# Kernel optimization log

Measured on AMD Instinct MI355X. Metric: run time of the kernel, lower is better.

The kernel has to match this reference:

```python
import jax, jax.numpy as jnp
import numpy as np

B, N, D, H, DEPTH = 2, 2048, 768, 12, 4
DH = D // H
SCALE = DH ** -0.5
EPS = 1e-5
FF = 4 * D


def layer_norm(x, w, b):
    m = jnp.mean(x, axis=-1, keepdims=True)
    v = jnp.mean((x - m) ** 2, axis=-1, keepdims=True)
    return (x - m) * jax.lax.rsqrt(v + EPS) * w + b


def to_heads(t):  # [b, n, D] -> [b, H, n, DH]
    b, n, _ = t.shape
    return t.reshape(b, n, H, DH).transpose(0, 2, 1, 3)


def merge_heads(t):  # [b, H, n, DH] -> [b, n, D]
    b, h, n, dh = t.shape
    return t.transpose(0, 2, 1, 3).reshape(b, n, D)


def attend(q, k, v, bias):
    s = jnp.einsum('bhid,bhjd->bhij', q, k) * SCALE + bias
    a = jax.nn.softmax(s, axis=-1)
    return merge_heads(jnp.einsum('bhij,bhjd->bhid', a, v))


def setup_inputs():
    key = jax.random.key(0)
    ks = iter(jax.random.split(key, 16))

    def p(shape, scale=0.02):
        return jax.random.normal(next(ks), shape, dtype=jnp.float32) * scale

    inp = {
        'x': jax.random.normal(next(ks), (B, N, D), dtype=jnp.float32),
        'context': jax.random.normal(next(ks), (B, N, D), dtype=jnp.float32),
        'relative_position_bias': jax.random.normal(next(ks), (1, H, N, N), dtype=jnp.float32) * 0.02,
        # self-attn params (stacked over depth)
        'ln1_w': jnp.ones((DEPTH, D), jnp.float32), 'ln1_b': jnp.zeros((DEPTH, D), jnp.float32),
        'w_qkv': p((DEPTH, D, 3 * D)),
        'w_so': p((DEPTH, D, D)), 'b_so': jnp.zeros((DEPTH, D), jnp.float32),
        # cross-attn params (shared LN applied to x and context, as in source)
        'ln2_w': jnp.ones((DEPTH, D), jnp.float32), 'ln2_b': jnp.zeros((DEPTH, D), jnp.float32),
        'w_q': p((DEPTH, D, D)), 'w_k': p((DEPTH, D, D)), 'w_v': p((DEPTH, D, D)),
        'w_co': p((DEPTH, D, D)), 'b_co': jnp.zeros((DEPTH, D), jnp.float32),
        # FFN params
        'ln3_w': jnp.ones((DEPTH, D), jnp.float32), 'ln3_b': jnp.zeros((DEPTH, D), jnp.float32),
        'w_f1': p((DEPTH, D, FF)), 'b_f1': jnp.zeros((DEPTH, FF), jnp.float32),
        'w_f2': p((DEPTH, FF, D)), 'b_f2': jnp.zeros((DEPTH, D), jnp.float32),
        # final norm
        'lnout_w': jnp.ones((D,), jnp.float32), 'lnout_b': jnp.zeros((D,), jnp.float32),
    }
    return inp


def reference(x, context, relative_position_bias,
              ln1_w, ln1_b, w_qkv, w_so, b_so,
              ln2_w, ln2_b, w_q, w_k, w_v, w_co, b_co,
              ln3_w, ln3_b, w_f1, b_f1, w_f2, b_f2,
              lnout_w, lnout_b):
    bias = relative_position_bias
    for i in range(DEPTH):
        # self-attention block (pre-norm, residual)
        xn = layer_norm(x, ln1_w[i], ln1_b[i])
        q, k, v = jnp.split(xn @ w_qkv[i], 3, axis=-1)
        o = attend(to_heads(q), to_heads(k), to_heads(v), bias)
        x = o @ w_so[i] + b_so[i] + x
        # cross-attention block (input_norm shared for x and context)
        xn = layer_norm(x, ln2_w[i], ln2_b[i])
        cn = layer_norm(context, ln2_w[i], ln2_b[i])
        o = attend(to_heads(xn @ w_q[i]), to_heads(cn @ w_k[i]), to_heads(cn @ w_v[i]), bias)
        x = o @ w_co[i] + b_co[i] + x
        # FFN block
        xn = layer_norm(x, ln3_w[i], ln3_b[i])
        h = jax.nn.gelu(xn @ w_f1[i] + b_f1[i], approximate=False)
        x = h @ w_f2[i] + b_f2[i] + x
    return layer_norm(x, lnout_w, lnout_b)
```

## Files before the change

### kernel.cpp

```cpp
#include <hip/hip_runtime.h>
#include <cstdint>
#include <cstddef>

#define DEV static __device__ __forceinline__

typedef float  f32x4 __attribute__((ext_vector_type(4)));
typedef short  s16x8 __attribute__((ext_vector_type(8)));
typedef unsigned short u16;
typedef unsigned short u16x2 __attribute__((ext_vector_type(2)));
typedef unsigned short u16x4 __attribute__((ext_vector_type(4)));
typedef __bf16 bf16x8 __attribute__((ext_vector_type(8)));

#define LOG2E 1.4426950408889634f
#define QSCALE_CONST 0.18033688011112042f

DEV float bf2f(u16 v){ union { unsigned u; float f; } x; x.u = ((unsigned)v) << 16; return x.f; }
DEV u16 f2bf(float f){ return __builtin_bit_cast(u16, (__bf16)f); }

DEV float fexp2(float x){
#if __has_builtin(__builtin_amdgcn_exp2f)
  return __builtin_amdgcn_exp2f(x);
#else
  return exp2f(x);
#endif
}

DEV f32x4 mfma16(s16x8 a, s16x8 b, f32x4 c){
  return __builtin_amdgcn_mfma_f32_16x16x32_bf16(
      __builtin_bit_cast(bf16x8, a), __builtin_bit_cast(bf16x8, b), c, 0, 0, 0);
}

DEV void gld16(const void* g, void* l){
  __builtin_amdgcn_global_load_lds(
      (const __attribute__((address_space(1))) void*)(uintptr_t)g,
      (__attribute__((address_space(3))) void*)(unsigned)(uintptr_t)l,
      16, 0, 0);
}

__global__ void __launch_bounds__(256)
transpose_cvt(const float* __restrict__ src, u16* __restrict__ dst, int K, int N,
              size_t dzstride){
  int z = blockIdx.z;
  src += (size_t)z * K * N;
  dst += (size_t)z * dzstride;
  __shared__ float t[32][33];
  int n0 = blockIdx.x * 32, k0 = blockIdx.y * 32;
#pragma unroll
  for (int i = 0; i < 4; ++i)
    t[threadIdx.y + 8*i][threadIdx.x] = src[(size_t)(k0 + threadIdx.y + 8*i) * N + n0 + threadIdx.x];
  __syncthreads();
#pragma unroll
  for (int i = 0; i < 4; ++i)
    dst[(size_t)(n0 + threadIdx.y + 8*i) * K + k0 + threadIdx.x] = f2bf(t[threadIdx.x][threadIdx.y + 8*i]);
}

__global__ void __launch_bounds__(256)
cvt_bias(const float* __restrict__ in, u16* __restrict__ out){
  size_t i = ((size_t)blockIdx.x * 256 + threadIdx.x) * 4;
  f32x4 v = *(const f32x4*)(in + i);
  u16x4 o;
#pragma unroll
  for (int j = 0; j < 4; ++j) o[j] = f2bf(v[j] * LOG2E);
  *(u16x4*)(out + i) = o;
}

template<typename OUT>
__global__ void __launch_bounds__(256)
ln_kernel(const float* __restrict__ x0, const float* __restrict__ x1,
          const float* __restrict__ w, const float* __restrict__ bsh,
          OUT* __restrict__ o0, OUT* __restrict__ o1){
  int row = blockIdx.x, tid = threadIdx.x;
  const float* xr; OUT* orow;
  if (row < 4096){ xr = x0 + (size_t)row * 768; orow = o0 + (size_t)row * 768; }
  else           { xr = x1 + (size_t)(row - 4096) * 768; orow = o1 + (size_t)(row - 4096) * 768; }
  float v0 = xr[tid], v1 = xr[tid + 256], v2 = xr[tid + 512];
  float s = v0 + v1 + v2, s2 = v0*v0 + v1*v1 + v2*v2;
#pragma unroll
  for (int off = 1; off < 64; off <<= 1){ s += __shfl_xor(s, off); s2 += __shfl_xor(s2, off); }
  __shared__ float red[8];
  int wid = tid >> 6;
  if ((tid & 63) == 0){ red[wid] = s; red[wid + 4] = s2; }
  __syncthreads();
  s  = red[0] + red[1] + red[2] + red[3];
  s2 = red[4] + red[5] + red[6] + red[7];
  float m = s * (1.f/768.f);
  float var = s2 * (1.f/768.f) - m * m;
  float rstd = rsqrtf(var + 1e-5f);
#pragma unroll
  for (int i = 0; i < 3; ++i){
    int c = tid + 256 * i;
    float vv = (i == 0 ? v0 : (i == 1 ? v1 : v2));
    float o = (vv - m) * rstd * w[c] + bsh[c];
    if constexpr (sizeof(OUT) == 2) orow[c] = f2bf(o);
    else                            orow[c] = o;
  }
}

template<int BN, int EPI>
__global__ void __launch_bounds__(256)
gemm_bf16(const u16* __restrict__ A, int lda, const u16* __restrict__ Bt, int ldb,
          int nk, u16* __restrict__ Cb, float* __restrict__ Cf, int ldc,
          const float* __restrict__ bias, const float* __restrict__ resid){
  constexpr int NT = BN / 32;
  __shared__ u16 As[2][128 * 32];
  __shared__ u16 Bs[2][BN * 32];
  const int tid = threadIdx.x, w = tid >> 6, lane = tid & 63;
  const int l16 = lane & 15, g = lane >> 4;
  const int m0 = blockIdx.x * 128, n0 = blockIdx.y * BN;
  const int wm = (w >> 1) * 64, wn = (w & 1) * (BN / 2);
  f32x4 acc[4][NT] = {};

  const int L0 = w * 1024 + lane * 16;
  const int L1 = (w + 4) * 1024 + lane * 16;
  const u16* a0 = A + (size_t)(m0 + (L0 >> 6)) * lda + ((L0 & 63) >> 1);
  const u16* a1 = A + (size_t)(m0 + (L1 >> 6)) * lda + ((L1 & 63) >> 1);
  const u16* b0; const u16* b1 = nullptr;
  if constexpr (BN == 128){
    b0 = Bt + (size_t)(n0 + (L0 >> 6)) * ldb + ((L0 & 63) >> 1);
    b1 = Bt + (size_t)(n0 + (L1 >> 6)) * ldb + ((L1 & 63) >> 1);
  } else {
    const int Lb = tid * 16;
    b0 = Bt + (size_t)(n0 + (Lb >> 6)) * ldb + ((Lb & 63) >> 1);
  }

  {
    char* ab = (char*)As[0]; char* bb = (char*)Bs[0];
    gld16(a0, ab + w * 1024); gld16(a1, ab + (w + 4) * 1024);
    if constexpr (BN == 128){ gld16(b0, bb + w * 1024); gld16(b1, bb + (w + 4) * 1024); }
    else                    { gld16(b0, bb + w * 1024); }
  }
  __syncthreads();

  int cb = 0;
  for (int kt = 0; kt < nk; ++kt){
    if (kt + 1 < nk){
      const int k1 = (kt + 1) * 32;
      char* ab = (char*)As[cb ^ 1]; char* bb = (char*)Bs[cb ^ 1];
      gld16(a0 + k1, ab + w * 1024); gld16(a1 + k1, ab + (w + 4) * 1024);
      if constexpr (BN == 128){ gld16(b0 + k1, bb + w * 1024); gld16(b1 + k1, bb + (w + 4) * 1024); }
      else                    { gld16(b0 + k1, bb + w * 1024); }
    }

    const u16* Ab = As[cb]; const u16* Bb = Bs[cb];
    s16x8 af[4], bfv[NT];
#pragma unroll
    for (int mi = 0; mi < 4; ++mi)
      af[mi] = *(const s16x8*)(Ab + (wm + mi*16 + l16) * 32 + 8 * g);
#pragma unroll
    for (int ni = 0; ni < NT; ++ni)
      bfv[ni] = *(const s16x8*)(Bb + (wn + ni*16 + l16) * 32 + 8 * g);
#pragma unroll
    for (int mi = 0; mi < 4; ++mi)
#pragma unroll
      for (int ni = 0; ni < NT; ++ni)
        acc[mi][ni] = mfma16(af[mi], bfv[ni], acc[mi][ni]);

    __syncthreads();
    cb ^= 1;
  }

#pragma unroll
  for (int mi = 0; mi < 4; ++mi){
    const int rg = m0 + wm + mi*16 + 4*g;
#pragma unroll
    for (int ni = 0; ni < NT; ++ni){
      const int col = n0 + wn + ni*16 + l16;
      f32x4 v = acc[mi][ni];
#pragma unroll
      for (int r = 0; r < 4; ++r){
        const int row = rg + r;
        if constexpr (EPI == 0){
          Cb[(size_t)row * ldc + col] = f2bf(v[r]);
        } else if constexpr (EPI == 1){
          Cf[(size_t)row * ldc + col] = v[r] + bias[col] + resid[(size_t)row * ldc + col];
        } else if constexpr (EPI == 2){
          float t = v[r] + bias[col];
          float ge = 0.5f * t * (1.0f + erff(t * 0.7071067811865476f));
          Cb[(size_t)row * ldc + col] = f2bf(ge);
        } else {
          float sc = (col < 768) ? QSCALE_CONST : 1.0f;
          Cb[(size_t)row * ldc + col] = f2bf(v[r] * sc);
        }
      }
    }
  }
}

__global__ void __launch_bounds__(256)
attn_kernel(const u16* __restrict__ qkv, const u16* __restrict__ bias, u16* __restrict__ out){
  __shared__ __align__(16) u16 Ks [2 * 4096];
  __shared__ __align__(16) u16 Bsh[2 * 4096];
  __shared__ __align__(16) u16 Vt [4096];
  __shared__ __align__(16) u16 Pl [4 * 1024];

  const int tid = threadIdx.x, w = tid >> 6, lane = tid & 63;
  const int l16 = lane & 15, g = lane >> 4;
  const int qt = blockIdx.x, h = blockIdx.y, b = blockIdx.z;
  const int rowbase = b * 2048, q0 = qt * 64;

  const int ci0 = w * 64 + lane, ci1 = ci0 + 256;
  const int r0 = ci0 >> 3, sc0 = ci0 & 7, r1 = ci1 >> 3, sc1 = ci1 & 7;
  const u16* kp0 = qkv + (size_t)(rowbase + r0) * 2304 + 768 + h * 64 + (((sc0 ^ (r0 & 7)) & 7) << 3);
  const u16* kp1 = qkv + (size_t)(rowbase + r1) * 2304 + 768 + h * 64 + (((sc1 ^ (r1 & 7)) & 7) << 3);
  const u16* bp0 = bias + ((size_t)h * 2048 + q0 + r0) * 2048 + (((sc0 ^ (r0 & 7)) & 7) << 3);
  const u16* bp1 = bias + ((size_t)h * 2048 + q0 + r1) * 2048 + (((sc1 ^ (r1 & 7)) & 7) << 3);
  const int dh0 = (tid & 31) * 2, vs = tid >> 5;
  const u16* vp = qkv + (size_t)(rowbase + vs * 8) * 2304 + 1536 + h * 64 + dh0;
  u16x2 vr[8];

  const u16* qrow = qkv + (size_t)(rowbase + q0 + w * 16 + l16) * 2304 + h * 64;
  s16x8 qf0 = *(const s16x8*)(qrow + 8 * g);
  s16x8 qf1 = *(const s16x8*)(qrow + 32 + 8 * g);

  f32x4 oacc[4] = {};
  float mrun = -3.0e38f, lrun = 0.f;
  const int sw = l16 & 7;

  {
    char* kb = (char*)Ks + w * 1024;
    gld16(kp0, kb); gld16(kp1, kb + 4096);
    char* bb = (char*)Bsh + w * 1024;
    gld16(bp0, bb); gld16(bp1, bb + 4096);
#pragma unroll
    for (int i = 0; i < 8; ++i) vr[i] = *(const u16x2*)(vp + (size_t)i * 2304);
  }
  __syncthreads();
  {
    s16x8 vA, vB;
#pragma unroll
    for (int j = 0; j < 8; ++j){ vA[j] = (short)vr[j][0]; vB[j] = (short)vr[j][1]; }
    *(s16x8*)(Vt + dh0 * 64 + ((vs ^ (dh0 & 7)) << 3)) = vA;
    *(s16x8*)(Vt + (dh0 + 1) * 64 + ((vs ^ ((dh0 + 1) & 7)) << 3)) = vB;
  }
  __syncthreads();

  int cb = 0;
  for (int t = 0; t < 32; ++t){
    if (t < 31){
      const size_t koff = (size_t)(t + 1) * 64 * 2304;
      char* kb = (char*)Ks + (cb ^ 1) * 8192 + w * 1024;
      gld16(kp0 + koff, kb); gld16(kp1 + koff, kb + 4096);
      char* bb = (char*)Bsh + (cb ^ 1) * 8192 + w * 1024;
      gld16(bp0 + (t + 1) * 64, bb); gld16(bp1 + (t + 1) * 64, bb + 4096);
      const u16* p = vp + koff;
#pragma unroll
      for (int i = 0; i < 8; ++i) vr[i] = *(const u16x2*)(p + (size_t)i * 2304);
    }

    const u16* Kb = Ks + cb * 4096;
    const u16* Bb = Bsh + cb * 4096;

    f32x4 st[4];
#pragma unroll
    for (int mi = 0; mi < 4; ++mi){
      const int row = l16 + 16 * mi;
      s16x8 kf0 = *(const s16x8*)(Kb + row * 64 + ((g ^ sw) << 3));
      s16x8 kf1 = *(const s16x8*)(Kb + row * 64 + (((g + 4) ^ sw) << 3));
      f32x4 z = {};
      z = mfma16(kf0, qf0, z);
      st[mi] = mfma16(kf1, qf1, z);
    }

    const int brow = w * 16 + l16;
    float tmax = -3.0e38f;
#pragma unroll
    for (int mi = 0; mi < 4; ++mi){
      u16x4 bb = *(const u16x4*)(Bb + brow * 64 + (((2*mi + (g >> 1)) ^ sw) << 3) + 4 * (g & 1));
#pragma unroll
      for (int r = 0; r < 4; ++r){
        float v = st[mi][r] + bf2f(bb[r]);
        st[mi][r] = v;
        tmax = fmaxf(tmax, v);
      }
    }
    tmax = fmaxf(tmax, __shfl_xor(tmax, 16));
    tmax = fmaxf(tmax, __shfl_xor(tmax, 32));
    if (!__all(tmax <= mrun + 8.f)){
      float mnew = fmaxf(mrun, tmax);
      float al = fexp2(mrun - mnew);
      mrun = mnew;
      lrun *= al;
#pragma unroll
      for (int r = 0; r < 4; ++r){
        float aq = __shfl(al, 4 * g + r);
#pragma unroll
        for (int ni = 0; ni < 4; ++ni) oacc[ni][r] *= aq;
      }
    }
    float ssum = 0.f;
#pragma unroll
    for (int mi = 0; mi < 4; ++mi){
      u16x4 pk;
#pragma unroll
      for (int r = 0; r < 4; ++r){
        float pv = fexp2(st[mi][r] - mrun);
        ssum += pv;
        pk[r] = f2bf(pv);
      }
      *(u16x4*)(Pl + w * 1024 + l16 * 64 + (((2*mi + (g >> 1)) ^ sw) << 3) + 4 * (g & 1)) = pk;
    }
    ssum += __shfl_xor(ssum, 16);
    ssum += __shfl_xor(ssum, 32);
    lrun += ssum;

#pragma unroll
    for (int ks2 = 0; ks2 < 2; ++ks2){
      s16x8 pf = *(const s16x8*)(Pl + w * 1024 + l16 * 64 + (((4*ks2 + g) ^ sw) << 3));
#pragma unroll
      for (int ni = 0; ni < 4; ++ni){
        const int dh = l16 + 16 * ni;
        s16x8 vf = *(const s16x8*)(Vt + dh * 64 + (((4*ks2 + g) ^ sw) << 3));
        oacc[ni] = mfma16(pf, vf, oacc[ni]);
      }
    }

    __syncthreads();
    if (t < 31){
      s16x8 vA, vB;
#pragma unroll
      for (int j = 0; j < 8; ++j){ vA[j] = (short)vr[j][0]; vB[j] = (short)vr[j][1]; }
      *(s16x8*)(Vt + dh0 * 64 + ((vs ^ (dh0 & 7)) << 3)) = vA;
      *(s16x8*)(Vt + (dh0 + 1) * 64 + ((vs ^ ((dh0 + 1) & 7)) << 3)) = vB;
    }
    __syncthreads();
    cb ^= 1;
  }

#pragma unroll
  for (int r = 0; r < 4; ++r){
    float lq = __shfl(lrun, 4 * g + r);
    float inv = 1.0f / lq;
    const int row = rowbase + q0 + w * 16 + 4 * g + r;
#pragma unroll
    for (int ni = 0; ni < 4; ++ni)
      out[(size_t)row * 768 + h * 64 + l16 + 16 * ni] = f2bf(oacc[ni][r] * inv);
  }
}

extern "C" void kernel_launch(void* const* d_in, const int* in_sizes, int n_in,
                              void* d_out, int out_size, void* d_ws, size_t ws_size,
                              hipStream_t stream){
  const float* in_x    = (const float*)d_in[0];
  const float* in_ctx  = (const float*)d_in[1];
  const float* in_bias = (const float*)d_in[2];
  const float* ln1_w = (const float*)d_in[3];
  const float* ln1_b = (const float*)d_in[4];
  const float* w_qkv = (const float*)d_in[5];
  const float* w_so  = (const float*)d_in[6];
  const float* b_so  = (const float*)d_in[7];
  const float* ln2_w = (const float*)d_in[8];
  const float* ln2_b = (const float*)d_in[9];
  const float* w_q   = (const float*)d_in[10];
  const float* w_k   = (const float*)d_in[11];
  const float* w_v   = (const float*)d_in[12];
  const float* w_co  = (const float*)d_in[13];
  const float* b_co  = (const float*)d_in[14];
  const float* ln3_w = (const float*)d_in[15];
  const float* ln3_b = (const float*)d_in[16];
  const float* w_f1  = (const float*)d_in[17];
  const float* b_f1  = (const float*)d_in[18];
  const float* w_f2  = (const float*)d_in[19];
  const float* b_f2  = (const float*)d_in[20];
  const float* lnout_w = (const float*)d_in[21];
  const float* lnout_b = (const float*)d_in[22];

  char* p = (char*)d_ws;
  float* xbuf  = (float*)p;  p += 4096ll * 768 * 4;
  u16* xn      = (u16*)p;    p += 4096ll * 768 * 2;
  u16* cn      = (u16*)p;    p += 4096ll * 768 * 2;
  u16* qkvb    = (u16*)p;    p += 4096ll * 2304 * 2;
  u16* attO    = (u16*)p;    p += 4096ll * 768 * 2;
  u16* ffh     = (u16*)p;    p += 4096ll * 3072 * 2;
  u16* wqkvT   = (u16*)p;    p += 4ll * 2304 * 768 * 2;
  u16* wsoT    = (u16*)p;    p += 4ll * 768 * 768 * 2;
  u16* wqT     = (u16*)p;    p += 4ll * 768 * 768 * 2;
  u16* wkvT    = (u16*)p;    p += 4ll * 1536 * 768 * 2;
  u16* wcoT    = (u16*)p;    p += 4ll * 768 * 768 * 2;
  u16* wf1T    = (u16*)p;    p += 4ll * 3072 * 768 * 2;
  u16* wf2T    = (u16*)p;    p += 4ll * 768 * 3072 * 2;
  u16* biasbf  = (u16*)p;    p += 12ll * 2048 * 2048 * 2;

  hipMemcpyAsync(xbuf, in_x, 4096ll * 768 * 4, hipMemcpyDeviceToDevice, stream);

  const dim3 tb(32, 8);
  transpose_cvt<<<dim3(72, 24, 4), tb, 0, stream>>>(w_qkv, wqkvT, 768, 2304, 2304ll*768);
  transpose_cvt<<<dim3(24, 24, 4), tb, 0, stream>>>(w_so,  wsoT,  768, 768,  768ll*768);
  transpose_cvt<<<dim3(24, 24, 4), tb, 0, stream>>>(w_q,   wqT,   768, 768,  768ll*768);
  transpose_cvt<<<dim3(24, 24, 4), tb, 0, stream>>>(w_k,   wkvT,             768, 768, 1536ll*768);
  transpose_cvt<<<dim3(24, 24, 4), tb, 0, stream>>>(w_v,   wkvT + 768ll*768, 768, 768, 1536ll*768);
  transpose_cvt<<<dim3(24, 24, 4), tb, 0, stream>>>(w_co,  wcoT,  768, 768,  768ll*768);
  transpose_cvt<<<dim3(96, 24, 4), tb, 0, stream>>>(w_f1,  wf1T,  768, 3072, 3072ll*768);
  transpose_cvt<<<dim3(24, 96, 4), tb, 0, stream>>>(w_f2,  wf2T,  3072, 768, 768ll*3072);
  cvt_bias<<<49152, 256, 0, stream>>>(in_bias, biasbf);

  const dim3 ag(32, 12, 2);
  for (int i = 0; i < 4; ++i){
    ln_kernel<u16><<<4096, 256, 0, stream>>>(xbuf, nullptr, ln1_w + i*768, ln1_b + i*768, xn, nullptr);
    gemm_bf16<128,3><<<dim3(32, 18), 256, 0, stream>>>(xn, 768, wqkvT + (size_t)i*2304*768, 768, 24,
                                                       qkvb, nullptr, 2304, nullptr, nullptr);
    attn_kernel<<<ag, 256, 0, stream>>>(qkvb, biasbf, attO);
    gemm_bf16<64,1><<<dim3(32, 12), 256, 0, stream>>>(attO, 768, wsoT + (size_t)i*768*768, 768, 24,
                                                      nullptr, xbuf, 768, b_so + i*768, xbuf);
    ln_kernel<u16><<<8192, 256, 0, stream>>>(xbuf, in_ctx, ln2_w + i*768, ln2_b + i*768, xn, cn);
    gemm_bf16<64,3><<<dim3(32, 12), 256, 0, stream>>>(xn, 768, wqT + (size_t)i*768*768, 768, 24,
                                                      qkvb, nullptr, 2304, nullptr, nullptr);
    gemm_bf16<64,0><<<dim3(32, 24), 256, 0, stream>>>(cn, 768, wkvT + (size_t)i*1536*768, 768, 24,
                                                      qkvb + 768, nullptr, 2304, nullptr, nullptr);
    attn_kernel<<<ag, 256, 0, stream>>>(qkvb, biasbf, attO);
    gemm_bf16<64,1><<<dim3(32, 12), 256, 0, stream>>>(attO, 768, wcoT + (size_t)i*768*768, 768, 24,
                                                      nullptr, xbuf, 768, b_co + i*768, xbuf);
    ln_kernel<u16><<<4096, 256, 0, stream>>>(xbuf, nullptr, ln3_w + i*768, ln3_b + i*768, xn, nullptr);
    gemm_bf16<128,2><<<dim3(32, 24), 256, 0, stream>>>(xn, 768, wf1T + (size_t)i*3072*768, 768, 24,
                                                       ffh, nullptr, 3072, b_f1 + i*3072, nullptr);
    gemm_bf16<64,1><<<dim3(32, 12), 256, 0, stream>>>(ffh, 3072, wf2T + (size_t)i*768*3072, 3072, 96,
                                                      nullptr, xbuf, 768, b_f2 + i*768, xbuf);
  }
  ln_kernel<float><<<4096, 256, 0, stream>>>(xbuf, nullptr, lnout_w, lnout_b, (float*)d_out, nullptr);
}
```

Measured before the change: 1.481 ms.

## Double-buffer V, load bias into registers, merge cross-attn Q/KV GEMMs

The attention kernel now reads the relative-position bias straight from global memory into registers in its MFMA output layout, instead of staging it through shared memory. V is double-buffered in LDS, which removes one of the two block barriers per key tile. The cross-attention Q and K/V projections are merged into one GEMM launch that uses blockIdx.z to pick the operands and the output offset. This cuts LDS traffic, barriers and one launch per layer, at the cost of more registers and uncoalesced 8-byte bias loads.

```diff
diff --git a/kernel.cpp b/kernel.cpp
--- a/kernel.cpp
+++ b/kernel.cpp
@@ -100,10 +100,18 @@
 __global__ void __launch_bounds__(256)
 gemm_bf16(const u16* __restrict__ A, int lda, const u16* __restrict__ Bt, int ldb,
           int nk, u16* __restrict__ Cb, float* __restrict__ Cf, int ldc,
-          const float* __restrict__ bias, const float* __restrict__ resid){
+          const float* __restrict__ bias, const float* __restrict__ resid,
+          const u16* __restrict__ A2, const u16* __restrict__ Bt2){
   constexpr int NT = BN / 32;
   __shared__ u16 As[2][128 * 32];
   __shared__ u16 Bs[2][BN * 32];
+  float colscale = 1.0f;
+  if constexpr (EPI == 4){
+    const int z = blockIdx.z;
+    if (z == 0){ colscale = QSCALE_CONST; }
+    else { A = A2; Bt = Bt2 + (size_t)(z - 1) * 768 * 768; }
+    Cb += z * 768;
+  }
   const int tid = threadIdx.x, w = tid >> 6, lane = tid & 63;
   const int l16 = lane & 15, g = lane >> 4;
   const int m0 = blockIdx.x * 128, n0 = blockIdx.y * BN;
@@ -177,9 +185,11 @@
           float t = v[r] + bias[col];
           float ge = 0.5f * t * (1.0f + erff(t * 0.7071067811865476f));
           Cb[(size_t)row * ldc + col] = f2bf(ge);
-        } else {
+        } else if constexpr (EPI == 3){
           float sc = (col < 768) ? QSCALE_CONST : 1.0f;
           Cb[(size_t)row * ldc + col] = f2bf(v[r] * sc);
+        } else {
+          Cb[(size_t)row * ldc + col] = f2bf(v[r] * colscale);
         }
       }
     }
@@ -188,10 +198,9 @@
 
 __global__ void __launch_bounds__(256)
 attn_kernel(const u16* __restrict__ qkv, const u16* __restrict__ bias, u16* __restrict__ out){
-  __shared__ __align__(16) u16 Ks [2 * 4096];
-  __shared__ __align__(16) u16 Bsh[2 * 4096];
-  __shared__ __align__(16) u16 Vt [4096];
-  __shared__ __align__(16) u16 Pl [4 * 1024];
+  __shared__ __align__(16) u16 Ks[2][4096];
+  __shared__ __align__(16) u16 Vt[2][4096];
+  __shared__ __align__(16) u16 Pl[4][1024];
 
   const int tid = threadIdx.x, w = tid >> 6, lane = tid & 63;
   const int l16 = lane & 15, g = lane >> 4;
@@ -202,11 +211,11 @@
   const int r0 = ci0 >> 3, sc0 = ci0 & 7, r1 = ci1 >> 3, sc1 = ci1 & 7;
   const u16* kp0 = qkv + (size_t)(rowbase + r0) * 2304 + 768 + h * 64 + (((sc0 ^ (r0 & 7)) & 7) << 3);
   const u16* kp1 = qkv + (size_t)(rowbase + r1) * 2304 + 768 + h * 64 + (((sc1 ^ (r1 & 7)) & 7) << 3);
-  const u16* bp0 = bias + ((size_t)h * 2048 + q0 + r0) * 2048 + (((sc0 ^ (r0 & 7)) & 7) << 3);
-  const u16* bp1 = bias + ((size_t)h * 2048 + q0 + r1) * 2048 + (((sc1 ^ (r1 & 7)) & 7) << 3);
   const int dh0 = (tid & 31) * 2, vs = tid >> 5;
   const u16* vp = qkv + (size_t)(rowbase + vs * 8) * 2304 + 1536 + h * 64 + dh0;
   u16x2 vr[8];
+  const u16* bptr = bias + ((size_t)h * 2048 + q0 + w * 16 + l16) * 2048 + 4 * g;
+  u16x4 brc[4], brn[4];
 
   const u16* qrow = qkv + (size_t)(rowbase + q0 + w * 16 + l16) * 2304 + h * 64;
   s16x8 qf0 = *(const s16x8*)(qrow + 8 * g);
@@ -217,58 +226,51 @@
   const int sw = l16 & 7;
 
   {
-    char* kb = (char*)Ks + w * 1024;
+    char* kb = (char*)Ks[0] + w * 1024;
     gld16(kp0, kb); gld16(kp1, kb + 4096);
-    char* bb = (char*)Bsh + w * 1024;
-    gld16(bp0, bb); gld16(bp1, bb + 4096);
 #pragma unroll
     for (int i = 0; i < 8; ++i) vr[i] = *(const u16x2*)(vp + (size_t)i * 2304);
+#pragma unroll
+    for (int mi = 0; mi < 4; ++mi) brc[mi] = *(const u16x4*)(bptr + 16 * mi);
+    s16x8 vA, vB;
+#pragma unroll
+    for (int j = 0; j < 8; ++j){ vA[j] = (short)vr[j][0]; vB[j] = (short)vr[j][1]; }
+    *(s16x8*)(Vt[0] + dh0 * 64 + ((vs ^ (dh0 & 7)) << 3)) = vA;
+    *(s16x8*)(Vt[0] + (dh0 + 1) * 64 + ((vs ^ ((dh0 + 1) & 7)) << 3)) = vB;
   }
   __syncthreads();
-  {
-    s16x8 vA, vB;
-#pragma unroll
-    for (int j = 0; j < 8; ++j){ vA[j] = (short)vr[j][0]; vB[j] = (short)vr[j][1]; }
-    *(s16x8*)(Vt + dh0 * 64 + ((vs ^ (dh0 & 7)) << 3)) = vA;
-    *(s16x8*)(Vt + (dh0 + 1) * 64 + ((vs ^ ((dh0 + 1) & 7)) << 3)) = vB;
-  }
-  __syncthreads();
-
-  int cb = 0;
+
   for (int t = 0; t < 32; ++t){
+    const int cb = t & 1;
     if (t < 31){
       const size_t koff = (size_t)(t + 1) * 64 * 2304;
-      char* kb = (char*)Ks + (cb ^ 1) * 8192 + w * 1024;
+      char* kb = (char*)Ks[cb ^ 1] + w * 1024;
       gld16(kp0 + koff, kb); gld16(kp1 + koff, kb + 4096);
-      char* bb = (char*)Bsh + (cb ^ 1) * 8192 + w * 1024;
-      gld16(bp0 + (t + 1) * 64, bb); gld16(bp1 + (t + 1) * 64, bb + 4096);
       const u16* p = vp + koff;
 #pragma unroll
       for (int i = 0; i < 8; ++i) vr[i] = *(const u16x2*)(p + (size_t)i * 2304);
-    }
-
-    const u16* Kb = Ks + cb * 4096;
-    const u16* Bb = Bsh + cb * 4096;
+      const u16* bp = bptr + (t + 1) * 64;
+#pragma unroll
+      for (int mi = 0; mi < 4; ++mi) brn[mi] = *(const u16x4*)(bp + 16 * mi);
+    }
 
     f32x4 st[4];
 #pragma unroll
     for (int mi = 0; mi < 4; ++mi){
       const int row = l16 + 16 * mi;
-      s16x8 kf0 = *(const s16x8*)(Kb + row * 64 + ((g ^ sw) << 3));
-      s16x8 kf1 = *(const s16x8*)(Kb + row * 64 + (((g + 4) ^ sw) << 3));
+      s16x8 kf0 = *(const s16x8*)(Ks[cb] + row * 64 + ((g ^ sw) << 3));
+      s16x8 kf1 = *(const s16x8*)(Ks[cb] + row * 64 + (((g + 4) ^ sw) << 3));
       f32x4 z = {};
       z = mfma16(kf0, qf0, z);
       st[mi] = mfma16(kf1, qf1, z);
     }
 
-    const int brow = w * 16 + l16;
     float tmax = -3.0e38f;
 #pragma unroll
     for (int mi = 0; mi < 4; ++mi){
-      u16x4 bb = *(const u16x4*)(Bb + brow * 64 + (((2*mi + (g >> 1)) ^ sw) << 3) + 4 * (g & 1));
 #pragma unroll
       for (int r = 0; r < 4; ++r){
-        float v = st[mi][r] + bf2f(bb[r]);
+        float v = st[mi][r] + bf2f(brc[mi][r]);
         st[mi][r] = v;
         tmax = fmaxf(tmax, v);
       }
@@ -297,7 +299,7 @@
         ssum += pv;
         pk[r] = f2bf(pv);
       }
-      *(u16x4*)(Pl + w * 1024 + l16 * 64 + (((2*mi + (g >> 1)) ^ sw) << 3) + 4 * (g & 1)) = pk;
+      *(u16x4*)(Pl[w] + l16 * 64 + (((2*mi + (g >> 1)) ^ sw) << 3) + 4 * (g & 1)) = pk;
     }
     ssum += __shfl_xor(ssum, 16);
     ssum += __shfl_xor(ssum, 32);
@@ -305,25 +307,25 @@
 
 #pragma unroll
     for (int ks2 = 0; ks2 < 2; ++ks2){
-      s16x8 pf = *(const s16x8*)(Pl + w * 1024 + l16 * 64 + (((4*ks2 + g) ^ sw) << 3));
+      s16x8 pf = *(const s16x8*)(Pl[w] + l16 * 64 + (((4*ks2 + g) ^ sw) << 3));
 #pragma unroll
       for (int ni = 0; ni < 4; ++ni){
         const int dh = l16 + 16 * ni;
-        s16x8 vf = *(const s16x8*)(Vt + dh * 64 + (((4*ks2 + g) ^ sw) << 3));
+        s16x8 vf = *(const s16x8*)(Vt[cb] + dh * 64 + (((4*ks2 + g) ^ sw) << 3));
         oacc[ni] = mfma16(pf, vf, oacc[ni]);
       }
     }
 
-    __syncthreads();
     if (t < 31){
       s16x8 vA, vB;
 #pragma unroll
       for (int j = 0; j < 8; ++j){ vA[j] = (short)vr[j][0]; vB[j] = (short)vr[j][1]; }
-      *(s16x8*)(Vt + dh0 * 64 + ((vs ^ (dh0 & 7)) << 3)) = vA;
-      *(s16x8*)(Vt + (dh0 + 1) * 64 + ((vs ^ ((dh0 + 1) & 7)) << 3)) = vB;
+      *(s16x8*)(Vt[cb ^ 1] + dh0 * 64 + ((vs ^ (dh0 & 7)) << 3)) = vA;
+      *(s16x8*)(Vt[cb ^ 1] + (dh0 + 1) * 64 + ((vs ^ ((dh0 + 1) & 7)) << 3)) = vB;
+#pragma unroll
+      for (int mi = 0; mi < 4; ++mi) brc[mi] = brn[mi];
     }
     __syncthreads();
-    cb ^= 1;
   }
 
 #pragma unroll
@@ -397,23 +399,22 @@
   for (int i = 0; i < 4; ++i){
     ln_kernel<u16><<<4096, 256, 0, stream>>>(xbuf, nullptr, ln1_w + i*768, ln1_b + i*768, xn, nullptr);
     gemm_bf16<128,3><<<dim3(32, 18), 256, 0, stream>>>(xn, 768, wqkvT + (size_t)i*2304*768, 768, 24,
-                                                       qkvb, nullptr, 2304, nullptr, nullptr);
+                                                       qkvb, nullptr, 2304, nullptr, nullptr, nullptr, nullptr);
     attn_kernel<<<ag, 256, 0, stream>>>(qkvb, biasbf, attO);
     gemm_bf16<64,1><<<dim3(32, 12), 256, 0, stream>>>(attO, 768, wsoT + (size_t)i*768*768, 768, 24,
-                                                      nullptr, xbuf, 768, b_so + i*768, xbuf);
+                                                      nullptr, xbuf, 768, b_so + i*768, xbuf, nullptr, nullptr);
     ln_kernel<u16><<<8192, 256, 0, stream>>>(xbuf, in_ctx, ln2_w + i*768, ln2_b + i*768, xn, cn);
-    gemm_bf16<64,3><<<dim3(32, 12), 256, 0, stream>>>(xn, 768, wqT + (size_t)i*768*768, 768, 24,
-                                                      qkvb, nullptr, 2304, nullptr, nullptr);
-    gemm_bf16<64,0><<<dim3(32, 24), 256, 0, stream>>>(cn, 768, wkvT + (size_t)i*1536*768, 768, 24,
-                                                      qkvb + 768, nullptr, 2304, nullptr, nullptr);
+    gemm_bf16<64,4><<<dim3(32, 12, 3), 256, 0, stream>>>(xn, 768, wqT + (size_t)i*768*768, 768, 24,
+                                                         qkvb, nullptr, 2304, nullptr, nullptr,
+                                                         cn, wkvT + (size_t)i*1536*768);
     attn_kernel<<<ag, 256, 0, stream>>>(qkvb, biasbf, attO);
     gemm_bf16<64,1><<<dim3(32, 12), 256, 0, stream>>>(attO, 768, wcoT + (size_t)i*768*768, 768, 24,
-                                                      nullptr, xbuf, 768, b_co + i*768, xbuf);
+                                                      nullptr, xbuf, 768, b_co + i*768, xbuf, nullptr, nullptr);
     ln_kernel<u16><<<4096, 256, 0, stream>>>(xbuf, nullptr, ln3_w + i*768, ln3_b + i*768, xn, nullptr);
     gemm_bf16<128,2><<<dim3(32, 24), 256, 0, stream>>>(xn, 768, wf1T + (size_t)i*3072*768, 768, 24,
-                                                       ffh, nullptr, 3072, b_f1 + i*3072, nullptr);
+                                                       ffh, nullptr, 3072, b_f1 + i*3072, nullptr, nullptr, nullptr);
     gemm_bf16<64,1><<<dim3(32, 12), 256, 0, stream>>>(ffh, 3072, wf2T + (size_t)i*768*3072, 3072, 96,
-                                                      nullptr, xbuf, 768, b_f2 + i*768, xbuf);
+                                                      nullptr, xbuf, 768, b_f2 + i*768, xbuf, nullptr, nullptr);
   }
   ln_kernel<float><<<4096, 256, 0, stream>>>(xbuf, nullptr, lnout_w, lnout_b, (float*)d_out, nullptr);
 }
```

Result: no change. 1.459 ms (median of 2 runs) (-1.5%).
